# Kernel optimization log

Measured on AMD Instinct MI355X. Metric: run time of the kernel, lower is better.

Reference implementation:

```python
import jax, jax.numpy as jnp
import numpy as np

KH, KW = 7, 7
H, W = 4096, 4096

def setup_inputs() -> dict:
    key = jax.random.key(0)
    k1, k2 = jax.random.split(key)
    x = jax.random.normal(k1, (H, W), dtype=jnp.float32)
    weight = jax.random.normal(k2, (KH, KW), dtype=jnp.float32) * 0.001
    bias = jnp.zeros((1,), dtype=jnp.float32)
    return {"x": x, "weight": weight, "bias": bias}

def reference(x, weight, bias):
    # Single-channel valid 2D cross-correlation + scalar bias.
    # lax.conv_general_dilated performs cross-correlation (no kernel flip),
    # matching the torch loop: res[i,j] = sum(x[i:i+kh, j:j+kw] * k).
    lhs = x[None, None, :, :]            # [N=1, C=1, H, W]
    rhs = weight[None, None, :, :]       # [O=1, I=1, kh, kw]
    out = jax.lax.conv_general_dilated(
        lhs, rhs,
        window_strides=(1, 1),
        padding="VALID",
        dimension_numbers=("NCHW", "OIHW", "NCHW"),
    )
    return out[0, 0] + bias[0]           # [H-kh+1, W-kw+1]
```

## Files before the change

kernel.cpp:

```cpp
#include <hip/hip_runtime.h>
#include <stdint.h>

#define IH 4096
#define IW 4096
#define OH 4090
#define OW 4090

#define TW 256
#define NW 4
#define RPW 32
#define RSTEP 4
#define NSTEP 8
#define WIN 10
#define RING 14
#define LW 272
#define YB (NW * RPW)

typedef float v2f __attribute__((ext_vector_type(2)));
typedef __attribute__((address_space(1))) void gas_void;
typedef __attribute__((address_space(3))) void las_void;


__device__ __forceinline__ void stage_row(const float* __restrict__ x,
                                          int iy, int slot, int tile_x0,
                                          float* ring, int tx)
{
    iy = iy < IH ? iy : IH - 1;
    const float* gr = x + ((size_t)iy << 12);
    const int c0 = tile_x0 + 4 * tx;
    float* lp = ring + slot * LW;
    __builtin_amdgcn_global_load_lds((gas_void*)(gr + c0), (las_void*)lp, 16, 0, 0);
    int c1 = tile_x0 + 256 + tx;
    c1 = c1 <= IW - 1 ? c1 : IW - 1;
    if (tx < 16)
        __builtin_amdgcn_global_load_lds((gas_void*)(gr + c1), (las_void*)(lp + 256), 4, 0, 0);
}

__global__ __launch_bounds__(256, 2) void conv7x7_wavering(
    const float* __restrict__ x,
    const float* __restrict__ w,
    const float* __restrict__ bias,
    float* __restrict__ out)
{
    __shared__ float smem[NW * RING * LW];

    const int tid = threadIdx.x;
    const int tx  = tid & 63;
    const int wv  = tid >> 6;

    int tile_x0 = blockIdx.x * TW;
    if (tile_x0 > OW - TW) tile_x0 = OW - TW;
    int y0 = blockIdx.y * YB;
    if (y0 > OH - YB) y0 = OH - YB;

    const int strip_y0 = y0 + RPW * wv;
    float* ring = smem + wv * (RING * LW);

    float wt[49];
#pragma unroll
    for (int k = 0; k < 49; ++k) wt[k] = w[k];
    const float b = bias[0];

#pragma unroll
    for (int r = 0; r < WIN; ++r)
        stage_row(x, strip_y0 + r, r, tile_x0, ring, tx);

    const int lx0 = 4 * tx;
    const int ox0 = tile_x0 + lx0;
    int base = 0;

#pragma unroll 1
    for (int s = 0; s < NSTEP; ++s) {
        if (s + 1 < NSTEP) {
#pragma unroll
            for (int j = 0; j < RSTEP; ++j) {
                int sl = base + WIN + j;
                if (sl >= RING) sl -= RING;
                stage_row(x, strip_y0 + RSTEP * s + WIN + j, sl, tile_x0, ring, tx);
            }
        }
        __builtin_amdgcn_sched_barrier(0);

        if (s == 0 || s == NSTEP - 1) {
            asm volatile("s_waitcnt vmcnt(8)" ::: "memory");
        } else {
            asm volatile("s_waitcnt vmcnt(16)" ::: "memory");
        }
        __builtin_amdgcn_sched_barrier(0);

        float acc[RSTEP][4];
#pragma unroll
        for (int r = 0; r < RSTEP; ++r)
#pragma unroll
            for (int c = 0; c < 4; ++c) acc[r][c] = b;

#pragma unroll
        for (int ir = 0; ir < WIN; ++ir) {
            int sl = base + ir;
            if (sl >= RING) sl -= RING;
            const float* srow = ring + sl * LW + lx0;
            const float4 q0 = *(const float4*)(srow);
            const float4 q1 = *(const float4*)(srow + 4);
            const float4 q2 = *(const float4*)(srow + 8);
            float rb[12];
            rb[0]=q0.x; rb[1]=q0.y; rb[2]=q0.z;  rb[3]=q0.w;
            rb[4]=q1.x; rb[5]=q1.y; rb[6]=q1.z;  rb[7]=q1.w;
            rb[8]=q2.x; rb[9]=q2.y; rb[10]=q2.z; rb[11]=q2.w;

#pragma unroll
            for (int ky = 0; ky < 7; ++ky) {
                const int ry = ir - ky;
                if (ry >= 0 && ry < RSTEP) {
#pragma unroll
                    for (int kx = 0; kx < 7; ++kx) {
                        const float ww = wt[ky * 7 + kx];
#pragma unroll
                        for (int c = 0; c < 4; ++c)
                            acc[ry][c] += ww * rb[kx + c];
                    }
                }
            }
        }

#pragma unroll
        for (int ry = 0; ry < RSTEP; ++ry) {
            const int oy = strip_y0 + RSTEP * s + ry;
            float* orow = out + (size_t)oy * OW + ox0;
            v2f v0 = { acc[ry][0], acc[ry][1] };
            v2f v1 = { acc[ry][2], acc[ry][3] };
            asm volatile("global_store_dwordx2 %0, %1, off"
                         :: "v"(orow), "v"(v0));
            asm volatile("global_store_dwordx2 %0, %1, off"
                         :: "v"(orow + 2), "v"(v1));
        }

        base += RSTEP;
        if (base >= RING) base -= RING;
    }
}

extern "C" void kernel_launch(void* const* d_in, const int* in_sizes, int n_in,
                              void* d_out, int out_size, void* d_ws, size_t ws_size,
                              hipStream_t stream) {
    const float* x    = (const float*)d_in[0];
    const float* w    = (const float*)d_in[1];
    const float* bias = (const float*)d_in[2];
    float* out        = (float*)d_out;

    dim3 grid((OW + TW - 1) / TW, 4096 / YB);
    conv7x7_wavering<<<grid, dim3(256), 0, stream>>>(x, w, bias, out);
}
```

Measured before the change: 132.1 us.

## Keep sliding 8-row window in registers, shrink strips and LDS ring, raise occupancy

Each wave now handles 16 output rows instead of 32 and keeps an 8-row sliding window of input in registers. Only two new rows are read from LDS per step, rather than re-reading the full 10-row window every 4 outputs. The LDS ring shrinks to 8 rows, and launch bounds go up to 4 blocks per CU. The steps are fully unrolled with hand-tuned vmcnt waits. In exchange, the 6-row halo is re-read more often in global memory because strips are shorter, and the register window adds pressure.

```diff
diff --git a/kernel.cpp b/kernel.cpp
--- a/kernel.cpp
+++ b/kernel.cpp
@@ -8,11 +8,8 @@
 
 #define TW 256
 #define NW 4
-#define RPW 32
-#define RSTEP 4
-#define NSTEP 8
-#define WIN 10
-#define RING 14
+#define RPW 16
+#define RING 8
 #define LW 272
 #define YB (NW * RPW)
 
@@ -32,11 +29,62 @@
     __builtin_amdgcn_global_load_lds((gas_void*)(gr + c0), (las_void*)lp, 16, 0, 0);
     int c1 = tile_x0 + 256 + tx;
     c1 = c1 <= IW - 1 ? c1 : IW - 1;
-    if (tx < 16)
+    if (tx < 8)
         __builtin_amdgcn_global_load_lds((gas_void*)(gr + c1), (las_void*)(lp + 256), 4, 0, 0);
 }
 
-__global__ __launch_bounds__(256, 2) void conv7x7_wavering(
+#define READROW(W, SPTR) do {                                        \
+    const float4 q0_ = *(const float4*)(SPTR);                       \
+    const float4 q1_ = *(const float4*)((SPTR) + 4);                 \
+    const float4 q2_ = *(const float4*)((SPTR) + 8);                 \
+    (W)[0]=q0_.x; (W)[1]=q0_.y; (W)[2]=q0_.z;  (W)[3]=q0_.w;         \
+    (W)[4]=q1_.x; (W)[5]=q1_.y; (W)[6]=q1_.z;  (W)[7]=q1_.w;         \
+    (W)[8]=q2_.x; (W)[9]=q2_.y; (W)[10]=q2_.z; (W)[11]=q2_.w;        \
+} while (0)
+
+#define VMWAIT(N) do {                                               \
+    asm volatile("s_waitcnt vmcnt(" #N ")" ::: "memory");            \
+    __builtin_amdgcn_sched_barrier(0);                               \
+} while (0)
+
+#define LGKM0 do {                                                   \
+    asm volatile("s_waitcnt lgkmcnt(0)" ::: "memory");               \
+    __builtin_amdgcn_sched_barrier(0);                               \
+} while (0)
+
+#define READ2(S) do {                                                \
+    READROW(win[(2*(S)+6) & 7], ring + ((2*(S)+6) & 7) * LW + lx0);  \
+    READROW(win[(2*(S)+7) & 7], ring + ((2*(S)+7) & 7) * LW + lx0);  \
+} while (0)
+
+#define STAGE2(S) do {                                               \
+    stage_row(x, strip_y0 + 2*(S) + 14, (2*(S)+14) & 7, tile_x0, ring, tx); \
+    stage_row(x, strip_y0 + 2*(S) + 15, (2*(S)+15) & 7, tile_x0, ring, tx); \
+    __builtin_amdgcn_sched_barrier(0);                               \
+} while (0)
+
+#define COMP2(S, A0, A1) do {                                        \
+    _Pragma("unroll") for (int c = 0; c < 4; ++c) { (A0)[c] = b; (A1)[c] = b; } \
+    _Pragma("unroll") for (int ky = 0; ky < 7; ++ky) {               \
+        _Pragma("unroll") for (int kx = 0; kx < 7; ++kx) {           \
+            const float ww_ = wt[ky * 7 + kx];                       \
+            _Pragma("unroll") for (int c = 0; c < 4; ++c) {          \
+                (A0)[c] += ww_ * win[(2*(S)+ky)   & 7][kx + c];      \
+                (A1)[c] += ww_ * win[(2*(S)+1+ky) & 7][kx + c];      \
+            } } } } while (0)
+
+#define ST2(S, A0, A1) do {                                          \
+    float* o0_ = out + (size_t)(strip_y0 + 2*(S))     * OW + ox0;    \
+    float* o1_ = out + (size_t)(strip_y0 + 2*(S) + 1) * OW + ox0;    \
+    v2f p0_ = { (A0)[0], (A0)[1] }, p1_ = { (A0)[2], (A0)[3] };      \
+    v2f p2_ = { (A1)[0], (A1)[1] }, p3_ = { (A1)[2], (A1)[3] };      \
+    asm volatile("global_store_dwordx2 %0, %1, off" :: "v"(o0_),     "v"(p0_)); \
+    asm volatile("global_store_dwordx2 %0, %1, off" :: "v"(o0_ + 2), "v"(p1_)); \
+    asm volatile("global_store_dwordx2 %0, %1, off" :: "v"(o1_),     "v"(p2_)); \
+    asm volatile("global_store_dwordx2 %0, %1, off" :: "v"(o1_ + 2), "v"(p3_)); \
+} while (0)
+
+__global__ __launch_bounds__(256, 4) void conv7x7_regwin(
     const float* __restrict__ x,
     const float* __restrict__ w,
     const float* __restrict__ bias,
@@ -61,82 +109,39 @@
     for (int k = 0; k < 49; ++k) wt[k] = w[k];
     const float b = bias[0];
 
-#pragma unroll
-    for (int r = 0; r < WIN; ++r)
-        stage_row(x, strip_y0 + r, r, tile_x0, ring, tx);
-
     const int lx0 = 4 * tx;
     const int ox0 = tile_x0 + lx0;
-    int base = 0;
-
-#pragma unroll 1
-    for (int s = 0; s < NSTEP; ++s) {
-        if (s + 1 < NSTEP) {
-#pragma unroll
-            for (int j = 0; j < RSTEP; ++j) {
-                int sl = base + WIN + j;
-                if (sl >= RING) sl -= RING;
-                stage_row(x, strip_y0 + RSTEP * s + WIN + j, sl, tile_x0, ring, tx);
-            }
-        }
-        __builtin_amdgcn_sched_barrier(0);
-
-        if (s == 0 || s == NSTEP - 1) {
-            asm volatile("s_waitcnt vmcnt(8)" ::: "memory");
-        } else {
-            asm volatile("s_waitcnt vmcnt(16)" ::: "memory");
-        }
-        __builtin_amdgcn_sched_barrier(0);
-
-        float acc[RSTEP][4];
-#pragma unroll
-        for (int r = 0; r < RSTEP; ++r)
-#pragma unroll
-            for (int c = 0; c < 4; ++c) acc[r][c] = b;
 
 #pragma unroll
-        for (int ir = 0; ir < WIN; ++ir) {
-            int sl = base + ir;
-            if (sl >= RING) sl -= RING;
-            const float* srow = ring + sl * LW + lx0;
-            const float4 q0 = *(const float4*)(srow);
-            const float4 q1 = *(const float4*)(srow + 4);
-            const float4 q2 = *(const float4*)(srow + 8);
-            float rb[12];
-            rb[0]=q0.x; rb[1]=q0.y; rb[2]=q0.z;  rb[3]=q0.w;
-            rb[4]=q1.x; rb[5]=q1.y; rb[6]=q1.z;  rb[7]=q1.w;
-            rb[8]=q2.x; rb[9]=q2.y; rb[10]=q2.z; rb[11]=q2.w;
+    for (int r = 0; r < 8; ++r)
+        stage_row(x, strip_y0 + r, r, tile_x0, ring, tx);
+    VMWAIT(0);
+
+    float win[8][12];
+#pragma unroll
+    for (int r = 0; r < 8; ++r)
+        READROW(win[r], ring + r * LW + lx0);
+    LGKM0;
 
 #pragma unroll
-            for (int ky = 0; ky < 7; ++ky) {
-                const int ry = ir - ky;
-                if (ry >= 0 && ry < RSTEP) {
-#pragma unroll
-                    for (int kx = 0; kx < 7; ++kx) {
-                        const float ww = wt[ky * 7 + kx];
-#pragma unroll
-                        for (int c = 0; c < 4; ++c)
-                            acc[ry][c] += ww * rb[kx + c];
-                    }
-                }
-            }
-        }
+    for (int r = 8; r < 14; ++r)
+        stage_row(x, strip_y0 + r, r & 7, tile_x0, ring, tx);
+    __builtin_amdgcn_sched_barrier(0);
 
-#pragma unroll
-        for (int ry = 0; ry < RSTEP; ++ry) {
-            const int oy = strip_y0 + RSTEP * s + ry;
-            float* orow = out + (size_t)oy * OW + ox0;
-            v2f v0 = { acc[ry][0], acc[ry][1] };
-            v2f v1 = { acc[ry][2], acc[ry][3] };
-            asm volatile("global_store_dwordx2 %0, %1, off"
-                         :: "v"(orow), "v"(v0));
-            asm volatile("global_store_dwordx2 %0, %1, off"
-                         :: "v"(orow + 2), "v"(v1));
-        }
+    float a0[4], a1[4];
 
-        base += RSTEP;
-        if (base >= RING) base -= RING;
-    }
+    COMP2(0, a0, a1);
+    LGKM0;
+    STAGE2(0);
+    ST2(0, a0, a1);
+
+    VMWAIT(16); READ2(1); COMP2(1, a0, a1); LGKM0; STAGE2(1); ST2(1, a0, a1);
+    VMWAIT(20); READ2(2); COMP2(2, a0, a1); LGKM0; STAGE2(2); ST2(2, a0, a1);
+    VMWAIT(24); READ2(3); COMP2(3, a0, a1); LGKM0; STAGE2(3); ST2(3, a0, a1);
+    VMWAIT(28); READ2(4); COMP2(4, a0, a1); LGKM0; ST2(4, a0, a1);
+    VMWAIT(24); READ2(5); COMP2(5, a0, a1); LGKM0; ST2(5, a0, a1);
+    VMWAIT(20); READ2(6); COMP2(6, a0, a1); LGKM0; ST2(6, a0, a1);
+    VMWAIT(16); READ2(7); COMP2(7, a0, a1); LGKM0; ST2(7, a0, a1);
 }
 
 extern "C" void kernel_launch(void* const* d_in, const int* in_sizes, int n_in,
@@ -148,5 +153,5 @@
     float* out        = (float*)d_out;
 
     dim3 grid((OW + TW - 1) / TW, 4096 / YB);
-    conv7x7_wavering<<<grid, dim3(256), 0, stream>>>(x, w, bias, out);
+    conv7x7_regwin<<<grid, dim3(256), 0, stream>>>(x, w, bias, out);
 }
```

Result: slower. 196.5 us (+48.8%).
